# Kernel optimization log

Hardware: AMD Instinct MI355X
Metric: run time of the kernel (lower is better)

Reference implementation:

```python
import jax, jax.numpy as jnp
import numpy as np

# dims
D_MODEL = 256; D_STATE = 16; D_CONV = 4; EXPAND = 2
D_INNER = D_MODEL * EXPAND            # 512
DT_RANK = 16                          # ceil(256/16)
B_SZ = 16; C_IN = 64; T_LR = 2560; R = 2; C_OUT = 64


def _p(key, shape, scale=0.02):
    return jax.random.normal(key, shape, jnp.float32) * scale


def setup_inputs() -> dict:
    key = jax.random.key(0)
    ks = iter(jax.random.split(key, 48))
    inp = {}
    inp['x'] = jax.random.normal(next(ks), (B_SZ, C_IN, T_LR), jnp.float32)
    # encoder: Conv1d(64->128,k3,p1) ; Conv1d(128->256,k3,p1)
    inp['enc_w1'] = _p(next(ks), (128, C_IN, 3)); inp['enc_b1'] = jnp.zeros((128,), jnp.float32)
    inp['enc_w2'] = _p(next(ks), (256, 128, 3)); inp['enc_b2'] = jnp.zeros((256,), jnp.float32)
    # BidirectionalMamba norms
    inp['norm1_w'] = jnp.ones((D_MODEL,), jnp.float32)
    inp['norm2_w'] = jnp.ones((D_MODEL,), jnp.float32)
    # one forward ('f') and one backward ('b') Mamba v1 block
    for p in ('f', 'b'):
        inp[p + '_inW'] = _p(next(ks), (2 * D_INNER, D_MODEL))
        inp[p + '_convW'] = _p(next(ks), (D_INNER, D_CONV), 0.2)
        inp[p + '_convb'] = jnp.zeros((D_INNER,), jnp.float32)
        inp[p + '_xW'] = _p(next(ks), (DT_RANK + 2 * D_STATE, D_INNER))
        inp[p + '_dtW'] = _p(next(ks), (D_INNER, DT_RANK), 0.1)
        inp[p + '_dtb'] = -4.0 + 2.0 * jax.random.uniform(next(ks), (D_INNER,), jnp.float32)
        inp[p + '_Alog'] = jnp.log(jnp.tile(jnp.arange(1, D_STATE + 1, dtype=jnp.float32), (D_INNER, 1)))
        inp[p + '_D'] = jnp.ones((D_INNER,), jnp.float32)
        inp[p + '_outW'] = _p(next(ks), (D_MODEL, D_INNER))
    # post-bottleneck: Conv1d(512->256,k3,p1) + BatchNorm1d(256) (eval)
    inp['convd_w'] = _p(next(ks), (256, 512, 3)); inp['convd_b'] = jnp.zeros((256,), jnp.float32)
    inp['bn_g'] = jnp.ones((256,), jnp.float32); inp['bn_b'] = jnp.zeros((256,), jnp.float32)
    inp['bn_mean'] = jnp.zeros((256,), jnp.float32); inp['bn_var'] = jnp.ones((256,), jnp.float32)
    # SubPixel1D: Conv1d(256 -> target_channels*r, k3, p1), r=2
    inp['sp_w'] = _p(next(ks), (C_OUT * R, 256, 3)); inp['sp_b'] = jnp.zeros((C_OUT * R,), jnp.float32)
    return inp


def silu(x):
    return x * jax.nn.sigmoid(x)


def conv1d(x, w, b):  # x: (B,C,L), w: (O,I,K), 'same' padding
    k = w.shape[-1]
    y = jax.lax.conv_general_dilated(x, w, (1,), [(k // 2, k // 2)],
                                     dimension_numbers=('NCH', 'OIH', 'NCH'))
    return y + b[None, :, None]


def rmsnorm(x, w, eps=1e-6):
    return x * jax.lax.rsqrt(jnp.mean(x * x, -1, keepdims=True) + eps) * w


def mamba(x, inW, convW, convb, xW, dtW, dtb, Alog, Dp, outW):
    # x: (B, L, D_MODEL) -> (B, L, D_MODEL); Mamba v1 selective scan.
    Bn = x.shape[0]
    xz = x @ inW.T                               # (B,L,2*di)
    xc, z = jnp.split(xz, 2, axis=-1)            # (B,L,di) each
    # causal depthwise conv over time
    xt = jnp.transpose(xc, (0, 2, 1))            # (B,di,L)
    xt = jax.lax.conv_general_dilated(xt, convW[:, None, :], (1,), [(D_CONV - 1, 0)],
                                      dimension_numbers=('NCH', 'OIH', 'NCH'),
                                      feature_group_count=D_INNER)
    xc = silu(jnp.transpose(xt + convb[None, :, None], (0, 2, 1)))  # (B,L,di)
    dbc = xc @ xW.T                              # (B,L,dt_rank+2N)
    dt = jax.nn.softplus(dbc[..., :DT_RANK] @ dtW.T + dtb)          # (B,L,di)
    Bc = dbc[..., DT_RANK:DT_RANK + D_STATE]     # (B,L,N)
    Cc = dbc[..., DT_RANK + D_STATE:]            # (B,L,N)
    A = -jnp.exp(Alog)                           # (di,N)

    def step(h, inp):
        dt_t, B_t, C_t, x_t = inp                # (B,di),(B,N),(B,N),(B,di)
        dA = jnp.exp(dt_t[..., None] * A)        # (B,di,N)
        h = dA * h + (dt_t * x_t)[..., None] * B_t[:, None, :]
        y = jnp.einsum('bdn,bn->bd', h, C_t)
        return h, y

    xs = (jnp.transpose(dt, (1, 0, 2)), jnp.transpose(Bc, (1, 0, 2)),
          jnp.transpose(Cc, (1, 0, 2)), jnp.transpose(xc, (1, 0, 2)))
    h0 = jnp.zeros((Bn, D_INNER, D_STATE), x.dtype)
    _, ys = jax.lax.scan(step, h0, xs)           # ys: (L,B,di)
    y = jnp.transpose(ys, (1, 0, 2)) + xc * Dp
    return (y * silu(z)) @ outW.T


def reference(x, enc_w1, enc_b1, enc_w2, enc_b2, norm1_w, norm2_w,
              f_inW, f_convW, f_convb, f_xW, f_dtW, f_dtb, f_Alog, f_D, f_outW,
              b_inW, b_convW, b_convb, b_xW, b_dtW, b_dtb, b_Alog, b_D, b_outW,
              convd_w, convd_b, bn_g, bn_b, bn_mean, bn_var, sp_w, sp_b):
    # encoder (dropout = identity in eval)
    e = silu(conv1d(x, enc_w1, enc_b1))
    e = silu(conv1d(e, enc_w2, enc_b2))          # (B,256,T)
    t = jnp.transpose(e, (0, 2, 1))              # (B,T,256)
    # Bi-Mamba bottleneck layer
    xn = rmsnorm(t, norm1_w)
    mo_f = mamba(xn, f_inW, f_convW, f_convb, f_xW, f_dtW, f_dtb, f_Alog, f_D, f_outW) + xn
    xb = xn[:, ::-1, :]
    mo_b = mamba(xb, b_inW, b_convW, b_convb, b_xW, b_dtW, b_dtb, b_Alog, b_D, b_outW) + xb
    mo_b = mo_b[:, ::-1, :]
    combined = rmsnorm(mo_f + mo_b, norm2_w)
    m = jnp.concatenate([combined, t], axis=-1)  # (B,T,512)
    m = jnp.transpose(m, (0, 2, 1))              # (B,512,T)
    # conv_d + BatchNorm1d (eval) + SiLU
    d = conv1d(m, convd_w, convd_b)
    d = (d - bn_mean[None, :, None]) * jax.lax.rsqrt(bn_var + 1e-5)[None, :, None] \
        * bn_g[None, :, None] + bn_b[None, :, None]
    d = silu(d)
    # SubPixel1D upsample x2
    s = conv1d(d, sp_w, sp_b)                    # (B, C_OUT*R, T)
    Bn, C, T = s.shape
    s = s.reshape(Bn, C // R, R, T).transpose(0, 1, 3, 2).reshape(Bn, C // R, T * R)
    return s                                      # (B, 64, 5120)
```

## Files before the change

kernel.cpp:

```cpp
#include <hip/hip_runtime.h>
#include <hip/hip_bf16.h>
#include <math.h>

#define B_SZ 16
#define T_LR 2560
#define BT (B_SZ * T_LR)
#define DM 256
#define DI 512
#define DS 16
#define DTR 16
#define CH 128
#define CH_LOG2 7
#define CLEN (T_LR / CH)

typedef __attribute__((ext_vector_type(8))) short bf16x8;
typedef __attribute__((ext_vector_type(4))) float f32x4;

__device__ __forceinline__ float silu_f(float x) {
    return x / (1.f + __expf(-x));
}
__device__ __forceinline__ unsigned short f2bf(float v) {
    __hip_bfloat16 h = __float2bfloat16(v);
    return *(unsigned short*)&h;
}
__device__ __forceinline__ float bf2f(unsigned short u) {
    union { unsigned int i; float f; } c;
    c.i = (unsigned int)u << 16;
    return c.f;
}
__device__ __forceinline__ int seqrev(int r) {
    int s = r / T_LR, t = r % T_LR;
    return s * T_LR + (T_LR - 1 - t);
}
__device__ __forceinline__ float softplus_f(float x) {
    return (x > 20.f) ? x : __logf(1.f + __expf(x));
}
__device__ __forceinline__ size_t wswz_idx(int tap, int n, int c, int N, int Kt) {
    return ((size_t)((tap * (N >> 4) + (n >> 4)) * (Kt >> 5) + (c >> 5)) << 9)
         + (size_t)((((c >> 3) & 3) * 16 + (n & 15)) * 8 + (c & 7));
}

__global__ __launch_bounds__(256) void k_prep(
    const float* __restrict__ enc_w1, const float* __restrict__ enc_w2,
    const float* __restrict__ convd_w, const float* __restrict__ sp_w,
    const float* __restrict__ convd_b, const float* __restrict__ bn_g,
    const float* __restrict__ bn_b, const float* __restrict__ bn_mean,
    const float* __restrict__ bn_var,
    const float* __restrict__ inW0, const float* __restrict__ inW1,
    const float* __restrict__ outW0, const float* __restrict__ outW1,
    const float* __restrict__ xW0, const float* __restrict__ xW1,
    const float* __restrict__ Alog0, const float* __restrict__ Alog1,
    const float* __restrict__ x,
    unsigned short* __restrict__ W1r, unsigned short* __restrict__ W2r,
    unsigned short* __restrict__ Wdr, unsigned short* __restrict__ Wspr,
    float* __restrict__ alpha, float* __restrict__ beta,
    unsigned short* __restrict__ inW_bf2, unsigned short* __restrict__ outW_bf2,
    unsigned short* __restrict__ xW_bc2, float* __restrict__ Aflag,
    unsigned short* __restrict__ xt)
{
    __shared__ float ts[32][33];
    __shared__ int s_ok;
    int blk = blockIdx.x;
    int tid = threadIdx.x;
    if (blk < 32) {
        int i = blk * 256 + tid;
        int n = i / 64, ci = i % 64;
        #pragma unroll
        for (int k = 0; k < 3; k++)
            W1r[wswz_idx(k, n, ci, 128, 64)] = f2bf(enc_w1[((size_t)n * 64 + ci) * 3 + k]);
    } else if (blk < 160) {
        int i = (blk - 32) * 256 + tid;
        int n = i / 128, ci = i % 128;
        #pragma unroll
        for (int k = 0; k < 3; k++)
            W2r[wswz_idx(k, n, ci, 256, 128)] = f2bf(enc_w2[((size_t)n * 128 + ci) * 3 + k]);
    } else if (blk < 672) {
        int i = (blk - 160) * 256 + tid;
        int n = i / 512, ci = i % 512;
        #pragma unroll
        for (int k = 0; k < 3; k++)
            Wdr[wswz_idx(k, n, ci, 256, 512)] = f2bf(convd_w[((size_t)n * 512 + ci) * 3 + k]);
    } else if (blk < 800) {
        int i = (blk - 672) * 256 + tid;
        int n = i / 256, ci = i % 256;
        #pragma unroll
        for (int k = 0; k < 3; k++)
            Wspr[wswz_idx(k, n, ci, 128, 256)] = f2bf(sp_w[((size_t)n * 256 + ci) * 3 + k]);
    } else if (blk < 801) {
        int c = tid;
        float a = bn_g[c] * rsqrtf(bn_var[c] + 1e-5f);
        alpha[c] = a;
        beta[c] = (convd_b[c] - bn_mean[c]) * a + bn_b[c];
    } else if (blk < 1825) {
        int i = (blk - 801) * 256 + tid;
        inW_bf2[i] = f2bf(inW0[i]);
        inW_bf2[262144 + i] = f2bf(inW1[i]);
    } else if (blk < 2337) {
        int i = (blk - 1825) * 256 + tid;
        outW_bf2[i] = f2bf(outW0[i]);
        outW_bf2[131072 + i] = f2bf(outW1[i]);
    } else if (blk < 2433) {
        int i = (blk - 2337) * 256 + tid;
        xW_bc2[i] = f2bf(xW0[i]);
        xW_bc2[24576 + i] = f2bf(xW1[i]);
    } else if (blk < 2434) {
        if (tid == 0) s_ok = 1;
        __syncthreads();
        int ok = 1;
        for (int i = tid; i < DI * DS; i += 256) {
            int d = i >> 4, n = i & 15;
            float a0f = __expf(Alog0[d * DS]);
            float anf = __expf(Alog0[d * DS + n]);
            if (fabsf(anf - (float)(n + 1) * a0f) > 1e-3f * (float)(n + 1)) ok = 0;
            float a0b = __expf(Alog1[d * DS]);
            float anb = __expf(Alog1[d * DS + n]);
            if (fabsf(anb - (float)(n + 1) * a0b) > 1e-3f * (float)(n + 1)) ok = 0;
        }
        if (!ok) atomicAnd(&s_ok, 0);
        __syncthreads();
        if (tid == 0) Aflag[0] = s_ok ? 1.f : 0.f;
    } else {
        int idx = blk - 2434;
        int t0 = (idx % 80) * 32;
        int c0 = ((idx / 80) & 1) * 32;
        int b = idx / 160;
        int tx = tid & 31, ty = tid >> 5;
        #pragma unroll
        for (int j = 0; j < 4; j++) {
            int c = c0 + ty + j * 8;
            ts[ty + j * 8][tx] = x[((size_t)b * 64 + c) * T_LR + t0 + tx];
        }
        __syncthreads();
        #pragma unroll
        for (int j = 0; j < 4; j++) {
            int t = t0 + ty + j * 8;
            xt[((size_t)b * T_LR + t) * 64 + c0 + tx] = f2bf(ts[tx][ty + j * 8]);
        }
    }
}

__global__ __launch_bounds__(256, 3) void k_conv3_bf(const unsigned short* __restrict__ A1, int K1,
                                                  const unsigned short* __restrict__ A2, int K2,
                                                  const unsigned short* __restrict__ Wz,
                                                  const float* __restrict__ alpha,
                                                  const float* __restrict__ beta,
                                                  float* __restrict__ outf,
                                                  unsigned short* __restrict__ outb,
                                                  int N, int dosilu, int pixsh) {
    int Kt = K1 + K2;
    __shared__ __align__(16) unsigned short smem[2 * 130 * 40];
    unsigned short (*As)[130][40] = (unsigned short (*)[130][40])smem;
    float* sC = (float*)smem;
    int tid = threadIdx.x;
    int wave = tid >> 6, lane = tid & 63;
    int wm = (wave >> 1) * 64, wn = (wave & 1) * 64;
    int m0 = blockIdx.x * 128, n0 = blockIdx.y * 128;
    int b = m0 / T_LR, t0 = m0 % T_LR;
    int q = lane >> 4, ml = lane & 15;
    int Nb16 = N >> 4, Kb32 = Kt >> 5;
    int nb0 = (n0 + wn) >> 4;
    const unsigned short* wl = Wz + (size_t)lane * 8;
    f32x4 acc[4][4] = {};
    int cq = tid & 3;
    int r0 = tid >> 2;
    int r1 = r0 + 64;
    int r2 = r0 + 128;
    bool has2 = (tid < 8);
    int ta0 = t0 - 1 + r0, ta1 = t0 - 1 + r1, ta2 = t0 - 1 + r2;
    bool va0 = (ta0 >= 0) && (ta0 < T_LR);
    bool va1 = (ta1 < T_LR);
    bool va2 = has2 && (ta2 < T_LR);
    uint4 v0, v1, v2;
    #define LOADA(vv, valid, t, col) { vv = make_uint4(0u,0u,0u,0u); if (valid) { \
        const unsigned short* src = ((col) < K1) \
            ? A1 + (size_t)(b * T_LR + (t)) * K1 + (col) \
            : A2 + (size_t)(b * T_LR + (t)) * K2 + ((col) - K1); \
        vv = *(const uint4*)src; } }
    LOADA(v0, va0, ta0, cq * 8);
    LOADA(v1, va1, ta1, cq * 8);
    LOADA(v2, va2, ta2, cq * 8);
    *(uint4*)&As[0][r0][cq * 8] = v0;
    *(uint4*)&As[0][r1][cq * 8] = v1;
    if (has2) *(uint4*)&As[0][r2][cq * 8] = v2;
    int nk = Kb32;
    for (int kk = 0; kk < nk; kk++) {
        __syncthreads();
        int cur = kk & 1;
        int k0 = kk << 5;
        if (kk + 1 < nk) {
            int col = k0 + 32 + cq * 8;
            LOADA(v0, va0, ta0, col);
            LOADA(v1, va1, ta1, col);
            LOADA(v2, va2, ta2, col);
        }
        #pragma unroll
        for (int tap = 0; tap < 3; tap++) {
            int tb = tap * Nb16 + nb0;
            bf16x8 bfr[4];
            #pragma unroll
            for (int ni = 0; ni < 4; ni++)
                bfr[ni] = *(const bf16x8*)(wl + ((size_t)((tb + ni) * Kb32 + kk) << 9));
            #pragma unroll
            for (int mi = 0; mi < 4; mi++) {
                bf16x8 af = *(const bf16x8*)&As[cur][wm + mi * 16 + ml + tap][q * 8];
                #pragma unroll
                for (int ni = 0; ni < 4; ni++)
                    acc[mi][ni] = __builtin_amdgcn_mfma_f32_16x16x32_bf16(af, bfr[ni], acc[mi][ni], 0, 0, 0);
            }
        }
        if (kk + 1 < nk) {
            *(uint4*)&As[cur ^ 1][r0][cq * 8] = v0;
            *(uint4*)&As[cur ^ 1][r1][cq * 8] = v1;
            if (has2) *(uint4*)&As[cur ^ 1][r2][cq * 8] = v2;
        }
    }
    #undef LOADA
    int rowoff = m0 - b * T_LR;
    #pragma unroll
    for (int p = 0; p < 4; p++) {
        __syncthreads();
        if ((wave >> 1) == (p >> 1)) {
            int mib = (p & 1) * 2;
            #pragma unroll
            for (int m2 = 0; m2 < 2; m2++) {
                int mi = mib + m2;
                int rl = mi * 16 + q * 4 - (p & 1) * 32;
                #pragma unroll
                for (int r = 0; r < 4; r++)
                    #pragma unroll
                    for (int ni = 0; ni < 4; ni++)
                        sC[(rl + r) * 140 + wn + ni * 16 + ml] = acc[mi][ni][r];
            }
        }
        __syncthreads();
        if (pixsh) {
            int row = tid & 31, c2g = tid >> 5;
            int t = rowoff + p * 32 + row;
            float* dst = outf + ((size_t)b * 64 * T_LR + t) * 2;
            #pragma unroll
            for (int j = 0; j < 8; j++) {
                int c2 = c2g + j * 8;
                float va = sC[row * 140 + 2 * c2]     + beta[2 * c2];
                float vb = sC[row * 140 + 2 * c2 + 1] + beta[2 * c2 + 1];
                *(float2*)&dst[(size_t)c2 * T_LR * 2] = make_float2(va, vb);
            }
        } else {
            #pragma unroll
            for (int gi = 0; gi < 2; gi++) {
                int g = tid + gi * 256;
                int row = g >> 4;
                int colg = (g & 15) * 8;
                int mr = m0 + p * 32 + row;
                const float* src = sC + row * 140 + colg;
                float vv[8];
                *(float4*)&vv[0] = *(const float4*)src;
                *(float4*)&vv[4] = *(const float4*)(src + 4);
                unsigned short ob[8];
                #pragma unroll
                for (int jj = 0; jj < 8; jj++) {
                    int col = n0 + colg + jj;
                    float a = alpha ? alpha[col] : 1.f;
                    float v = vv[jj] * a + beta[col];
                    if (dosilu) v = silu_f(v);
                    vv[jj] = v;
                    ob[jj] = f2bf(v);
                }
                if (outf) {
                    *(float4*)(outf + (size_t)mr * N + n0 + colg) = *(float4*)&vv[0];
                    *(float4*)(outf + (size_t)mr * N + n0 + colg + 4) = *(float4*)&vv[4];
                }
                if (outb)
                    *(uint4*)(outb + (size_t)mr * N + n0 + colg) = *(uint4*)ob;
            }
        }
    }
}

__global__ __launch_bounds__(256) void k_inproj_conv(const unsigned short* __restrict__ xn,
                                                     const unsigned short* __restrict__ inW2,
                                                     const float* __restrict__ cw0,
                                                     const float* __restrict__ cw1,
                                                     const float* __restrict__ cb0,
                                                     const float* __restrict__ cb1,
                                                     unsigned short* __restrict__ xcs,
                                                     long long dsXcs) {
    __shared__ unsigned short As[128][40];
    __shared__ unsigned short Bs[128][40];
    __shared__ unsigned short Ct[131][136];
    int dir = blockIdx.z;
    int arev = dir;
    const unsigned short* inW = inW2 + (size_t)dir * 1024 * DM;
    const float* cw = dir ? cw1 : cw0;
    const float* cb = dir ? cb1 : cb0;
    xcs += (size_t)dir * dsXcs;
    int tid = threadIdx.x;
    int wave = tid >> 6, lane = tid & 63;
    int wm = (wave >> 1) * 64, wn = (wave & 1) * 64;
    int m0 = blockIdx.x * 128, n0 = blockIdx.y * 128;
    int b = m0 / T_LR, t0 = m0 % T_LR;
    int sc = tid & 3, sr = tid >> 2;
    int ar0 = m0 + sr, ar1 = m0 + sr + 64;
    if (arev) { ar0 = seqrev(ar0); ar1 = seqrev(ar1); }
    const unsigned short* ap0 = xn + (size_t)ar0 * DM + sc * 8;
    const unsigned short* ap1 = xn + (size_t)ar1 * DM + sc * 8;
    const unsigned short* bp0 = inW + (size_t)(n0 + sr) * DM + sc * 8;
    const unsigned short* bp1 = inW + (size_t)(n0 + sr + 64) * DM + sc * 8;
    f32x4 acc[4][4] = {};
    int q = lane >> 4, ml = lane & 15;
    for (int k0 = 0; k0 < DM; k0 += 32) {
        uint4 a0 = *(const uint4*)(ap0 + k0);
        uint4 a1 = *(const uint4*)(ap1 + k0);
        uint4 b0 = *(const uint4*)(bp0 + k0);
        uint4 b1 = *(const uint4*)(bp1 + k0);
        __syncthreads();
        *(uint4*)&As[sr][sc * 8]      = a0;
        *(uint4*)&As[sr + 64][sc * 8] = a1;
        *(uint4*)&Bs[sr][sc * 8]      = b0;
        *(uint4*)&Bs[sr + 64][sc * 8] = b1;
        __syncthreads();
        bf16x8 af[4], bfr[4];
        #pragma unroll
        for (int mi = 0; mi < 4; mi++)
            af[mi] = *(const bf16x8*)&As[wm + mi * 16 + ml][q * 8];
        #pragma unroll
        for (int ni = 0; ni < 4; ni++)
            bfr[ni] = *(const bf16x8*)&Bs[wn + ni * 16 + ml][q * 8];
        #pragma unroll
        for (int mi = 0; mi < 4; mi++)
            #pragma unroll
            for (int ni = 0; ni < 4; ni++)
                acc[mi][ni] = __builtin_amdgcn_mfma_f32_16x16x32_bf16(af[mi], bfr[ni], acc[mi][ni], 0, 0, 0);
    }
    #pragma unroll
    for (int mi = 0; mi < 4; mi++)
        #pragma unroll
        for (int r = 0; r < 4; r++)
            #pragma unroll
            for (int ni = 0; ni < 4; ni++)
                Ct[3 + wm + mi * 16 + q * 4 + r][wn + ni * 16 + ml] = f2bf(acc[mi][ni][r]);
    for (int i = tid; i < 384; i += 256) {
        int hr = i >> 7, c = i & 127;
        int tr = t0 - 3 + hr;
        float v = 0.f;
        if (tr >= 0) {
            int src = b * T_LR + (arev ? (T_LR - 1 - tr) : tr);
            const unsigned short* xr = xn + (size_t)src * DM;
            const unsigned short* wr = inW + (size_t)(n0 + c) * DM;
            for (int k = 0; k < DM; k += 8) {
                uint4 xa = *(const uint4*)(xr + k);
                uint4 wa = *(const uint4*)(wr + k);
                const unsigned short* xs = (const unsigned short*)&xa;
                const unsigned short* wsp = (const unsigned short*)&wa;
                #pragma unroll
                for (int j = 0; j < 8; j++) v += bf2f(xs[j]) * bf2f(wsp[j]);
            }
        }
        Ct[hr][c] = f2bf(v);
    }
    __syncthreads();
    int col = tid & 127;
    int d = n0 + col;
    float w0 = cw[d * 4 + 0], w1 = cw[d * 4 + 1], w2 = cw[d * 4 + 2], w3 = cw[d * 4 + 3];
    float bi = cb[d];
    int rbase = tid >> 7;
    for (int j = 0; j < 64; j++) {
        int row = rbase + 2 * j;
        float v = bi + bf2f(Ct[row][col]) * w0 + bf2f(Ct[row + 1][col]) * w1
                     + bf2f(Ct[row + 2][col]) * w2 + bf2f(Ct[row + 3][col]) * w3;
        xcs[(size_t)(m0 + row) * DI + d] = f2bf(silu_f(v));
    }
}

__global__ __launch_bounds__(256) void k_rmsnorm(const float* __restrict__ in1,
                                                 const float* __restrict__ in2,
                                                 const float* __restrict__ w,
                                                 float* __restrict__ out,
                                                 unsigned short* __restrict__ out_bf,
                                                 int ntok) {
    int tok = (blockIdx.x * 256 + threadIdx.x) >> 6;
    int lane = threadIdx.x & 63;
    if (tok >= ntok) return;
    float4 v = ((const float4*)(in1 + (size_t)tok * DM))[lane];
    if (in2) {
        float4 u = ((const float4*)(in2 + (size_t)tok * DM))[lane];
        v.x += u.x; v.y += u.y; v.z += u.z; v.w += u.w;
    }
    float ss = v.x * v.x + v.y * v.y + v.z * v.z + v.w * v.w;
    #pragma unroll
    for (int off = 32; off > 0; off >>= 1) ss += __shfl_xor(ss, off);
    float sc = rsqrtf(ss * (1.f / 256.f) + 1e-6f);
    float4 wv = ((const float4*)w)[lane];
    float4 o;
    o.x = v.x * sc * wv.x; o.y = v.y * sc * wv.y;
    o.z = v.z * sc * wv.z; o.w = v.w * sc * wv.w;
    if (out) ((float4*)(out + (size_t)tok * DM))[lane] = o;
    if (out_bf) {
        ushort4 ob;
        ob.x = f2bf(o.x); ob.y = f2bf(o.y); ob.z = f2bf(o.z); ob.w = f2bf(o.w);
        ((ushort4*)(out_bf + (size_t)tok * DM))[lane] = ob;
    }
}

__global__ __launch_bounds__(256) void k_gemm_bf(const unsigned short* __restrict__ A, int lda, long long dsA,
                                                 const unsigned short* __restrict__ Bw, long long dsB,
                                                 float* Cf, long long dsCf, int ldc,
                                                 const float* __restrict__ res,
                                                 int K, int Nout, int crevmode) {
    __shared__ unsigned short As[128][40];
    __shared__ unsigned short Bs[128][40];
    int dir = blockIdx.z;
    A += (long long)dir * dsA;
    Bw += (long long)dir * dsB;
    Cf += (long long)dir * dsCf;
    int crev = (crevmode == 2) ? dir : crevmode;
    int tid = threadIdx.x;
    int wave = tid >> 6, lane = tid & 63;
    int wm = (wave >> 1) * 64, wn = (wave & 1) * 64;
    int m0 = blockIdx.x * 128, n0 = blockIdx.y * 128;
    int sc = tid & 3, sr = tid >> 2;
    const unsigned short* ap0 = A + (size_t)(m0 + sr) * lda + sc * 8;
    const unsigned short* ap1 = A + (size_t)(m0 + sr + 64) * lda + sc * 8;
    bool bv0 = (n0 + sr) < Nout;
    bool bv1 = (n0 + sr + 64) < Nout;
    const unsigned short* bp0 = Bw + (size_t)(n0 + sr) * K + sc * 8;
    const unsigned short* bp1 = Bw + (size_t)(n0 + sr + 64) * K + sc * 8;
    f32x4 acc[4][4] = {};
    int q = lane >> 4, ml = lane & 15;
    for (int k0 = 0; k0 < K; k0 += 32) {
        uint4 a0 = *(const uint4*)(ap0 + k0);
        uint4 a1 = *(const uint4*)(ap1 + k0);
        uint4 b0 = make_uint4(0u, 0u, 0u, 0u), b1 = make_uint4(0u, 0u, 0u, 0u);
        if (bv0) b0 = *(const uint4*)(bp0 + k0);
        if (bv1) b1 = *(const uint4*)(bp1 + k0);
        __syncthreads();
        *(uint4*)&As[sr][sc * 8]      = a0;
        *(uint4*)&As[sr + 64][sc * 8] = a1;
        *(uint4*)&Bs[sr][sc * 8]      = b0;
        *(uint4*)&Bs[sr + 64][sc * 8] = b1;
        __syncthreads();
        bf16x8 af[4], bfr[4];
        #pragma unroll
        for (int mi = 0; mi < 4; mi++)
            af[mi] = *(const bf16x8*)&As[wm + mi * 16 + ml][q * 8];
        #pragma unroll
        for (int ni = 0; ni < 4; ni++)
            bfr[ni] = *(const bf16x8*)&Bs[wn + ni * 16 + ml][q * 8];
        #pragma unroll
        for (int mi = 0; mi < 4; mi++)
            #pragma unroll
            for (int ni = 0; ni < 4; ni++)
                acc[mi][ni] = __builtin_amdgcn_mfma_f32_16x16x32_bf16(af[mi], bfr[ni], acc[mi][ni], 0, 0, 0);
    }
    #pragma unroll
    for (int mi = 0; mi < 4; mi++) {
        #pragma unroll
        for (int r = 0; r < 4; r++) {
            int mr = m0 + wm + mi * 16 + q * 4 + r;
            int orow = crev ? seqrev(mr) : mr;
            #pragma unroll
            for (int ni = 0; ni < 4; ni++) {
                int col = n0 + wn + ni * 16 + ml;
                if (col < Nout) {
                    float v = acc[mi][ni][r];
                    if (res) v += res[(size_t)orow * ldc + col];
                    Cf[(size_t)orow * ldc + col] = v;
                }
            }
        }
    }
}

__global__ __launch_bounds__(256) void k_gemm_bf_cb(const unsigned short* __restrict__ A, int lda,
                                                    const unsigned short* __restrict__ Bw, long long dsB,
                                                    unsigned short* __restrict__ Cb, int ldc, long long dsCb,
                                                    const unsigned short* __restrict__ gate, long long dsGate,
                                                    int K) {
    __shared__ __align__(16) unsigned short smem[2 * 128 * 40];
    unsigned short (*As)[40] = (unsigned short(*)[40])smem;
    unsigned short (*Bs)[40] = (unsigned short(*)[40])(smem + 128 * 40);
    float* sC = (float*)smem;
    int dir = blockIdx.z;
    int arev = dir;
    Bw += (long long)dir * dsB;
    Cb += (long long)dir * dsCb;
    gate += (long long)dir * dsGate;
    int tid = threadIdx.x;
    int wave = tid >> 6, lane = tid & 63;
    int wm = (wave >> 1) * 64, wn = (wave & 1) * 64;
    int m0 = blockIdx.x * 128, n0 = blockIdx.y * 128;
    int sc = tid & 3, sr = tid >> 2;
    int ar0 = m0 + sr, ar1 = m0 + sr + 64;
    if (arev) { ar0 = seqrev(ar0); ar1 = seqrev(ar1); }
    const unsigned short* ap0 = A + (size_t)ar0 * lda + sc * 8;
    const unsigned short* ap1 = A + (size_t)ar1 * lda + sc * 8;
    const unsigned short* bp0 = Bw + (size_t)(n0 + sr) * K + sc * 8;
    const unsigned short* bp1 = Bw + (size_t)(n0 + sr + 64) * K + sc * 8;
    f32x4 acc[4][4] = {};
    int q = lane >> 4, ml = lane & 15;
    for (int k0 = 0; k0 < K; k0 += 32) {
        uint4 a0 = *(const uint4*)(ap0 + k0);
        uint4 a1 = *(const uint4*)(ap1 + k0);
        uint4 b0 = *(const uint4*)(bp0 + k0);
        uint4 b1 = *(const uint4*)(bp1 + k0);
        __syncthreads();
        *(uint4*)&As[sr][sc * 8]      = a0;
        *(uint4*)&As[sr + 64][sc * 8] = a1;
        *(uint4*)&Bs[sr][sc * 8]      = b0;
        *(uint4*)&Bs[sr + 64][sc * 8] = b1;
        __syncthreads();
        bf16x8 af[4], bfr[4];
        #pragma unroll
        for (int mi = 0; mi < 4; mi++)
            af[mi] = *(const bf16x8*)&As[wm + mi * 16 + ml][q * 8];
        #pragma unroll
        for (int ni = 0; ni < 4; ni++)
            bfr[ni] = *(const bf16x8*)&Bs[wn + ni * 16 + ml][q * 8];
        #pragma unroll
        for (int mi = 0; mi < 4; mi++)
            #pragma unroll
            for (int ni = 0; ni < 4; ni++)
                acc[mi][ni] = __builtin_amdgcn_mfma_f32_16x16x32_bf16(af[mi], bfr[ni], acc[mi][ni], 0, 0, 0);
    }
    #pragma unroll
    for (int p = 0; p < 4; p++) {
        __syncthreads();
        if ((wave >> 1) == (p >> 1)) {
            int mib = (p & 1) * 2;
            #pragma unroll
            for (int m2 = 0; m2 < 2; m2++) {
                int mi = mib + m2;
                int rl = mi * 16 + q * 4 - (p & 1) * 32;
                #pragma unroll
                for (int r = 0; r < 4; r++)
                    #pragma unroll
                    for (int ni = 0; ni < 4; ni++)
                        sC[(rl + r) * 140 + wn + ni * 16 + ml] = acc[mi][ni][r];
            }
        }
        __syncthreads();
        #pragma unroll
        for (int gi = 0; gi < 2; gi++) {
            int g = tid + gi * 256;
            int row = g >> 4;
            int colg = (g & 15) * 8;
            int grow = m0 + p * 32 + row;
            const float* src = sC + row * 140 + colg;
            float4 v0 = *(const float4*)src;
            float4 v1 = *(const float4*)(src + 4);
            float vv[8] = {v0.x, v0.y, v0.z, v0.w, v1.x, v1.y, v1.z, v1.w};
            unsigned short gu[8];
            *(uint4*)gu = *(const uint4*)(gate + (size_t)grow * ldc + n0 + colg);
            unsigned short o[8];
            #pragma unroll
            for (int jj = 0; jj < 8; jj++) {
                float v = vv[jj];
                v = silu_f(v) * bf2f(gu[jj]);
                o[jj] = f2bf(v);
            }
            *(uint4*)(Cb + (size_t)grow * ldc + n0 + colg) = *(uint4*)o;
        }
    }
}

__global__ __launch_bounds__(256) void k_scan_p1(const unsigned short* __restrict__ x,
                                                 const float* __restrict__ db,
                                                 const float* __restrict__ dtW0, const float* __restrict__ dtW1,
                                                 const float* __restrict__ dtb0, const float* __restrict__ dtb1,
                                                 const float* __restrict__ Alog0, const float* __restrict__ Alog1,
                                                 const float* __restrict__ Aflag,
                                                 float* __restrict__ hS,
                                                 float* __restrict__ csum, int Bc) {
    __shared__ float dbs[CLEN * 48];
    int tid = threadIdx.x;
    int gid = blockIdx.x * 256 + tid;
    int d = gid & (DI - 1);
    int bcix = gid >> 9;
    int c = bcix & (CH - 1);
    int bl = bcix >> CH_LOG2;
    int dir = (bl >= Bc) ? 1 : 0;
    const float* dtW  = dir ? dtW1  : dtW0;
    const float* dtb  = dir ? dtb1  : dtb0;
    const float* Alog = dir ? Alog1 : Alog0;
    int tbase = c * CLEN;
    const float* dbp = db + ((size_t)bl * T_LR + tbase) * 48;
    if (tid < 240) *(float4*)&dbs[tid * 4] = *(const float4*)(dbp + tid * 4);
    bool fast = (Aflag[0] != 0.f);
    float A0 = -__expf(Alog[d * DS]);
    float Av[DS], h[DS];
    #pragma unroll
    for (int n = 0; n < DS; n++) h[n] = 0.f;
    if (!fast) {
        #pragma unroll
        for (int n = 0; n < DS; n++) Av[n] = -__expf(Alog[d * DS + n]);
    }
    const float4* wp = (const float4*)(dtW + d * 16);
    float4 w0 = wp[0], w1 = wp[1], w2 = wp[2], w3 = wp[3];
    float bias = dtb[d];
    const unsigned short* xp = x + ((size_t)bl * T_LR + tbase) * DI + d;
    float S = 0.f;
    __syncthreads();
    for (int t = 0; t < CLEN; t++) {
        const float* bc = dbs + t * 48;
        float dl = bias
            + bc[0] * w0.x + bc[1] * w0.y + bc[2] * w0.z + bc[3] * w0.w
            + bc[4] * w1.x + bc[5] * w1.y + bc[6] * w1.z + bc[7] * w1.w
            + bc[8] * w2.x + bc[9] * w2.y + bc[10] * w2.z + bc[11] * w2.w
            + bc[12] * w3.x + bc[13] * w3.y + bc[14] * w3.z + bc[15] * w3.w;
        float dtv = softplus_f(dl);
        float xv  = bf2f(xp[(size_t)t * DI]);
        float dtx = dtv * xv;
        S += dtv;
        if (fast) {
            float e1 = __expf(dtv * A0);
            float e = e1;
            #pragma unroll
            for (int n = 0; n < DS; n++) {
                h[n] = e * h[n] + dtx * bc[16 + n];
                e *= e1;
            }
        } else {
            #pragma unroll
            for (int n = 0; n < DS; n++)
                h[n] = __expf(dtv * Av[n]) * h[n] + dtx * bc[16 + n];
        }
    }
    float* hp = hS + (size_t)gid * DS;
    #pragma unroll
    for (int n = 0; n < DS; n++) hp[n] = h[n];
    csum[gid] = S;
}

__global__ __launch_bounds__(256) void k_scan_p2(float* __restrict__ hS,
                                                 const float* __restrict__ csum,
                                                 const float* __restrict__ Alog0,
                                                 const float* __restrict__ Alog1, int Bc) {
    int gid = blockIdx.x * 256 + threadIdx.x;
    int n = gid & (DS - 1);
    int d = (gid >> 4) & (DI - 1);
    int bl = gid >> 13;
    const float* Alog = (bl >= Bc) ? Alog1 : Alog0;
    float An = -__expf(Alog[d * DS + n]);
    float hs = 0.f;
    for (int c = 0; c < CH; c++) {
        size_t base = ((size_t)(bl * CH + c) * DI + d);
        float he = hS[base * DS + n];
        float S  = csum[base];
        hS[base * DS + n] = hs;
        hs = __expf(An * S) * hs + he;
    }
}

__global__ __launch_bounds__(256) void k_scan_p3(unsigned short* __restrict__ x,
                                                 const float* __restrict__ db,
                                                 const float* __restrict__ dtW0, const float* __restrict__ dtW1,
                                                 const float* __restrict__ dtb0, const float* __restrict__ dtb1,
                                                 const float* __restrict__ Alog0, const float* __restrict__ Alog1,
                                                 const float* __restrict__ Aflag,
                                                 const float* __restrict__ Dp0, const float* __restrict__ Dp1,
                                                 const float* __restrict__ hS, int Bc) {
    __shared__ float dbs[CLEN * 48];
    int tid = threadIdx.x;
    int gid = blockIdx.x * 256 + tid;
    int d = gid & (DI - 1);
    int bcix = gid >> 9;
    int c = bcix & (CH - 1);
    int bl = bcix >> CH_LOG2;
    int dir = (bl >= Bc) ? 1 : 0;
    const float* dtW  = dir ? dtW1  : dtW0;
    const float* dtb  = dir ? dtb1  : dtb0;
    const float* Alog = dir ? Alog1 : Alog0;
    const float* Dp   = dir ? Dp1   : Dp0;
    int tbase = c * CLEN;
    const float* dbp = db + ((size_t)bl * T_LR + tbase) * 48;
    if (tid < 240) *(float4*)&dbs[tid * 4] = *(const float4*)(dbp + tid * 4);
    bool fast = (Aflag[0] != 0.f);
    float A0 = -__expf(Alog[d * DS]);
    float Av[DS], h[DS];
    const float* hp = hS + (size_t)gid * DS;
    #pragma unroll
    for (int n = 0; n < DS; n++) h[n] = hp[n];
    if (!fast) {
        #pragma unroll
        for (int n = 0; n < DS; n++) Av[n] = -__expf(Alog[d * DS + n]);
    }
    const float4* wp = (const float4*)(dtW + d * 16);
    float4 w0 = wp[0], w1 = wp[1], w2 = wp[2], w3 = wp[3];
    float bias = dtb[d];
    float Dd = Dp[d];
    unsigned short* xp = x + ((size_t)bl * T_LR + tbase) * DI + d;
    __syncthreads();
    for (int t = 0; t < CLEN; t++) {
        const float* bc = dbs + t * 48;
        float dl = bias
            + bc[0] * w0.x + bc[1] * w0.y + bc[2] * w0.z + bc[3] * w0.w
            + bc[4] * w1.x + bc[5] * w1.y + bc[6] * w1.z + bc[7] * w1.w
            + bc[8] * w2.x + bc[9] * w2.y + bc[10] * w2.z + bc[11] * w2.w
            + bc[12] * w3.x + bc[13] * w3.y + bc[14] * w3.z + bc[15] * w3.w;
        float dtv = softplus_f(dl);
        float xv  = bf2f(xp[(size_t)t * DI]);
        float dtx = dtv * xv;
        float acc = 0.f;
        if (fast) {
            float e1 = __expf(dtv * A0);
            float e = e1;
            #pragma unroll
            for (int n = 0; n < DS; n++) {
                h[n] = e * h[n] + dtx * bc[16 + n];
                acc += h[n] * bc[32 + n];
                e *= e1;
            }
        } else {
            #pragma unroll
            for (int n = 0; n < DS; n++) {
                h[n] = __expf(dtv * Av[n]) * h[n] + dtx * bc[16 + n];
                acc += h[n] * bc[32 + n];
            }
        }
        xp[(size_t)t * DI] = f2bf(acc + xv * Dd);
    }
}

extern "C" void kernel_launch(void* const* d_in, const int* in_sizes, int n_in,
                              void* d_out, int out_size, void* d_ws, size_t ws_size,
                              hipStream_t stream) {
    const float* x       = (const float*)d_in[0];
    const float* enc_w1  = (const float*)d_in[1];
    const float* enc_b1  = (const float*)d_in[2];
    const float* enc_w2  = (const float*)d_in[3];
    const float* enc_b2  = (const float*)d_in[4];
    const float* norm1_w = (const float*)d_in[5];
    const float* norm2_w = (const float*)d_in[6];
    const float* convd_w = (const float*)d_in[25];
    const float* convd_b = (const float*)d_in[26];
    const float* bn_g    = (const float*)d_in[27];
    const float* bn_b    = (const float*)d_in[28];
    const float* bn_mean = (const float*)d_in[29];
    const float* bn_var  = (const float*)d_in[30];
    const float* sp_w    = (const float*)d_in[31];
    const float* sp_b    = (const float*)d_in[32];
    float* out = (float*)d_out;

    const float* inW0   = (const float*)d_in[7];
    const float* cw0    = (const float*)d_in[8];
    const float* cb0    = (const float*)d_in[9];
    const float* xW0    = (const float*)d_in[10];
    const float* dtW0   = (const float*)d_in[11];
    const float* dtb0   = (const float*)d_in[12];
    const float* Alog0  = (const float*)d_in[13];
    const float* Dp0    = (const float*)d_in[14];
    const float* outW0  = (const float*)d_in[15];
    const float* inW1   = (const float*)d_in[16];
    const float* cw1    = (const float*)d_in[17];
    const float* cb1    = (const float*)d_in[18];
    const float* xW1    = (const float*)d_in[19];
    const float* dtW1   = (const float*)d_in[20];
    const float* dtb1   = (const float*)d_in[21];
    const float* Alog1  = (const float*)d_in[22];
    const float* Dp1    = (const float*)d_in[23];
    const float* outW1  = (const float*)d_in[24];

    float* ws = (float*)d_ws;
    size_t availf = ws_size / sizeof(float);
    size_t o = 0;
    float* t_buf  = ws + o; o += (size_t)BT * DM;
    float* xn_buf = ws + o; o += (size_t)BT * DM;
    float* mo     = ws + o; o += (size_t)BT * DM;
    unsigned short* xn_bf = (unsigned short*)(ws + o); o += (size_t)BT * DM / 2;
    unsigned short* tb_bf = (unsigned short*)(ws + o); o += (size_t)BT * DM / 2;
    unsigned short* inW_bf2  = (unsigned short*)(ws + o); o += (size_t)1024 * DM;
    unsigned short* outW_bf2 = (unsigned short*)(ws + o); o += (size_t)DM * DI;
    unsigned short* xW_bc2   = (unsigned short*)(ws + o); o += (size_t)48 * DI;
    unsigned short* W1r  = (unsigned short*)(ws + o); o += (3 * 128 * 64) / 2;
    unsigned short* W2r  = (unsigned short*)(ws + o); o += (3 * 256 * 128) / 2;
    unsigned short* Wdr  = (unsigned short*)(ws + o); o += (3 * 256 * 512) / 2;
    unsigned short* Wspr = (unsigned short*)(ws + o); o += (3 * 128 * 256) / 2;
    float* alpha_d = ws + o; o += 256;
    float* beta_d  = ws + o; o += 256;
    float* Aflag_d = ws + o; o += 4;
    size_t persist = o;
    float* scratch = ws + persist;
    size_t scratch_avail = (availf > persist) ? (availf - persist) : 0;
    size_t per_b2 = 2 * ((size_t)T_LR * DI / 2 * 2 + (size_t)T_LR * 48
                         + (size_t)CH * DI * (DS + 1));
    int Bc = 16;
    while (Bc > 1 && (size_t)Bc * per_b2 > scratch_avail) Bc >>= 1;

    unsigned short* xt  = (unsigned short*)mo;
    unsigned short* e1t = (unsigned short*)(mo + (size_t)BT * 64 / 2);
    unsigned short* comb_bf = (unsigned short*)xn_buf;
    unsigned short* d_bf = (unsigned short*)mo;

    k_prep<<<4994, 256, 0, stream>>>(enc_w1, enc_w2, convd_w, sp_w,
                                     convd_b, bn_g, bn_b, bn_mean, bn_var,
                                     inW0, inW1, outW0, outW1, xW0, xW1,
                                     Alog0, Alog1,
                                     x, W1r, W2r, Wdr, Wspr, alpha_d, beta_d,
                                     inW_bf2, outW_bf2, xW_bc2, Aflag_d, xt);

    k_conv3_bf<<<dim3(BT / 128, 1), 256, 0, stream>>>(xt, 64, nullptr, 0, W1r,
                                                      nullptr, enc_b1, nullptr, e1t, 128, 1, 0);
    k_conv3_bf<<<dim3(BT / 128, 2), 256, 0, stream>>>(e1t, 128, nullptr, 0, W2r,
                                                      nullptr, enc_b2, t_buf, tb_bf, 256, 1, 0);
    k_rmsnorm<<<BT / 4, 256, 0, stream>>>(t_buf, nullptr, norm1_w, xn_buf, xn_bf, BT);

    long long dsMo1 = (long long)(t_buf - mo);
    for (int b0 = 0; b0 < B_SZ; b0 += Bc) {
        int Tc = Bc * T_LR;
        long long TcDI = (long long)Tc * DI;
        unsigned short* xcs = (unsigned short*)scratch;
        unsigned short* ygb = xcs + (size_t)2 * Tc * DI;
        float* db   = (float*)(ygb + (size_t)2 * Tc * DI);
        float* hS   = db + (size_t)2 * Tc * 48;
        float* csum = hS + (size_t)2 * Bc * CH * DI * DS;
        const float*          xnC  = xn_buf + (size_t)b0 * T_LR * DM;
        const unsigned short* xnbC = xn_bf  + (size_t)b0 * T_LR * DM;
        float*                moC  = mo     + (size_t)b0 * T_LR * DM;
        k_inproj_conv<<<dim3(Tc / 128, DI / 128, 2), 256, 0, stream>>>(
            xnbC, inW_bf2, cw0, cw1, cb0, cb1, xcs, TcDI);
        k_gemm_bf<<<dim3(Tc / 128, 1, 2), 256, 0, stream>>>(
            xcs, DI, TcDI, xW_bc2, (long long)48 * DI,
            db, (long long)Tc * 48, 48, nullptr, DI, 48, 0);
        k_scan_p1<<<(2 * Bc * CH * DI) / 256, 256, 0, stream>>>(
            xcs, db, dtW0, dtW1, dtb0, dtb1, Alog0, Alog1, Aflag_d, hS, csum, Bc);
        k_scan_p2<<<(2 * Bc * DI * DS) / 256, 256, 0, stream>>>(
            hS, csum, Alog0, Alog1, Bc);
        k_scan_p3<<<(2 * Bc * CH * DI) / 256, 256, 0, stream>>>(
            xcs, db, dtW0, dtW1, dtb0, dtb1, Alog0, Alog1, Aflag_d, Dp0, Dp1, hS, Bc);
        k_gemm_bf_cb<<<dim3(Tc / 128, DI / 128, 2), 256, 0, stream>>>(
            xnbC, DM, inW_bf2 + (size_t)DI * DM, (long long)1024 * DM,
            ygb, DI, TcDI, xcs, TcDI, DM);
        k_gemm_bf<<<dim3(Tc / 128, DM / 128, 2), 256, 0, stream>>>(
            ygb, DI, TcDI, outW_bf2, (long long)DM * DI,
            moC, dsMo1, DM, xnC, DI, DM, 2);
    }

    k_rmsnorm<<<BT / 4, 256, 0, stream>>>(mo, t_buf, norm2_w, nullptr, comb_bf, BT);
    k_conv3_bf<<<dim3(BT / 128, 2), 256, 0, stream>>>(comb_bf, 256, tb_bf, 256, Wdr,
                                                      alpha_d, beta_d, nullptr, d_bf, 256, 1, 0);
    k_conv3_bf<<<dim3(BT / 128, 1), 256, 0, stream>>>(d_bf, 256, nullptr, 0, Wspr,
                                                      nullptr, sp_b, out, nullptr, 128, 0, 1);
}
```

Baseline: 1.157 ms.

## Stage conv weight fragments into LDS via async global_load_lds double buffering

In the bf16 conv3 MFMA kernel, weight fragments are now copied into a double-buffered shared-memory tile using direct global-to-LDS loads issued by all waves. Previously each wave read its own weight fragments straight from global memory, so the two waves sharing a column group fetched the same data twice. The activation tile drops to a single buffer, which adds a second barrier per K step, and launch bounds fall from 3 to 2 blocks per CU to fit the larger shared-memory footprint. The intent is less redundant global traffic and better latency hiding for the weight stream, at the cost of occupancy and extra synchronisation.

```diff
diff --git a/kernel.cpp b/kernel.cpp
--- a/kernel.cpp
+++ b/kernel.cpp
@@ -139,7 +139,7 @@
     }
 }
 
-__global__ __launch_bounds__(256, 3) void k_conv3_bf(const unsigned short* __restrict__ A1, int K1,
+__global__ __launch_bounds__(256, 2) void k_conv3_bf(const unsigned short* __restrict__ A1, int K1,
                                                   const unsigned short* __restrict__ A2, int K2,
                                                   const unsigned short* __restrict__ Wz,
                                                   const float* __restrict__ alpha,
@@ -148,23 +148,22 @@
                                                   unsigned short* __restrict__ outb,
                                                   int N, int dosilu, int pixsh) {
     int Kt = K1 + K2;
-    __shared__ __align__(16) unsigned short smem[2 * 130 * 40];
-    unsigned short (*As)[130][40] = (unsigned short (*)[130][40])smem;
-    float* sC = (float*)smem;
+    __shared__ __align__(16) unsigned short sA[130][40];
+    __shared__ __align__(16) unsigned short sB[2][2][12][512];
+    float* sC = (float*)&sB[0][0][0][0];
     int tid = threadIdx.x;
     int wave = tid >> 6, lane = tid & 63;
-    int wm = (wave >> 1) * 64, wn = (wave & 1) * 64;
+    int wm = (wave >> 1) * 64, wg = wave & 1;
+    int wn = wg * 64;
     int m0 = blockIdx.x * 128, n0 = blockIdx.y * 128;
     int b = m0 / T_LR, t0 = m0 % T_LR;
     int q = lane >> 4, ml = lane & 15;
     int Nb16 = N >> 4, Kb32 = Kt >> 5;
-    int nb0 = (n0 + wn) >> 4;
-    const unsigned short* wl = Wz + (size_t)lane * 8;
+    int nb0 = n0 >> 4;
+    const unsigned short* wlane = Wz + (size_t)lane * 8;
     f32x4 acc[4][4] = {};
     int cq = tid & 3;
-    int r0 = tid >> 2;
-    int r1 = r0 + 64;
-    int r2 = r0 + 128;
+    int r0 = tid >> 2, r1 = r0 + 64, r2 = r0 + 128;
     bool has2 = (tid < 8);
     int ta0 = t0 - 1 + r0, ta1 = t0 - 1 + r1, ta2 = t0 - 1 + r2;
     bool va0 = (ta0 >= 0) && (ta0 < T_LR);
@@ -176,44 +175,55 @@
             ? A1 + (size_t)(b * T_LR + (t)) * K1 + (col) \
             : A2 + (size_t)(b * T_LR + (t)) * K2 + ((col) - K1); \
         vv = *(const uint4*)src; } }
+    #define ISSUEB(kk, buf) { \
+        _Pragma("unroll") \
+        for (int j = 0; j < 6; j++) { \
+            int f = wave * 6 + j; \
+            int g = (f >= 12) ? 1 : 0; \
+            int rem = f - g * 12; \
+            int tap = rem >> 2, ni = rem & 3; \
+            const unsigned short* gsrc = wlane + \
+                ((size_t)((tap * Nb16 + nb0 + g * 4 + ni) * Kb32 + (kk)) << 9); \
+            unsigned short* ldst = &sB[buf][g][tap * 4 + ni][0]; \
+            __builtin_amdgcn_global_load_lds( \
+                (const __attribute__((address_space(1))) unsigned int*)gsrc, \
+                (__attribute__((address_space(3))) unsigned int*)ldst, 16, 0, 0); \
+        } }
     LOADA(v0, va0, ta0, cq * 8);
     LOADA(v1, va1, ta1, cq * 8);
     LOADA(v2, va2, ta2, cq * 8);
-    *(uint4*)&As[0][r0][cq * 8] = v0;
-    *(uint4*)&As[0][r1][cq * 8] = v1;
-    if (has2) *(uint4*)&As[0][r2][cq * 8] = v2;
+    ISSUEB(0, 0);
     int nk = Kb32;
     for (int kk = 0; kk < nk; kk++) {
-        __syncthreads();
         int cur = kk & 1;
-        int k0 = kk << 5;
+        __syncthreads();
+        *(uint4*)&sA[r0][cq * 8] = v0;
+        *(uint4*)&sA[r1][cq * 8] = v1;
+        if (has2) *(uint4*)&sA[r2][cq * 8] = v2;
+        __syncthreads();
         if (kk + 1 < nk) {
-            int col = k0 + 32 + cq * 8;
+            int col = ((kk + 1) << 5) + cq * 8;
             LOADA(v0, va0, ta0, col);
             LOADA(v1, va1, ta1, col);
             LOADA(v2, va2, ta2, col);
+            ISSUEB(kk + 1, cur ^ 1);
         }
         #pragma unroll
         for (int tap = 0; tap < 3; tap++) {
-            int tb = tap * Nb16 + nb0;
             bf16x8 bfr[4];
             #pragma unroll
             for (int ni = 0; ni < 4; ni++)
-                bfr[ni] = *(const bf16x8*)(wl + ((size_t)((tb + ni) * Kb32 + kk) << 9));
+                bfr[ni] = *(const bf16x8*)&sB[cur][wg][tap * 4 + ni][lane * 8];
             #pragma unroll
             for (int mi = 0; mi < 4; mi++) {
-                bf16x8 af = *(const bf16x8*)&As[cur][wm + mi * 16 + ml + tap][q * 8];
+                bf16x8 af = *(const bf16x8*)&sA[wm + mi * 16 + ml + tap][q * 8];
                 #pragma unroll
                 for (int ni = 0; ni < 4; ni++)
                     acc[mi][ni] = __builtin_amdgcn_mfma_f32_16x16x32_bf16(af, bfr[ni], acc[mi][ni], 0, 0, 0);
             }
         }
-        if (kk + 1 < nk) {
-            *(uint4*)&As[cur ^ 1][r0][cq * 8] = v0;
-            *(uint4*)&As[cur ^ 1][r1][cq * 8] = v1;
-            if (has2) *(uint4*)&As[cur ^ 1][r2][cq * 8] = v2;
-        }
-    }
+    }
+    #undef ISSUEB
     #undef LOADA
     int rowoff = m0 - b * T_LR;
     #pragma unroll
```

New measurement: 1.167 ms. About the same (+0.8%).
